# Kernel optimization log

Measured on AMD Instinct MI355X. Metric: run time of the kernel, lower is better.

The kernel has to match this reference:

```python
import jax, jax.numpy as jnp
import numpy as np
from jax import lax

D_MODEL = 512
D_FIBER = 32
D_CONTROL = 64
MOMENTUM = 0.9


def setup_inputs() -> dict:
    key = jax.random.key(0)
    ks = jax.random.split(key, 7)
    B, S = 8, 4096
    hidden = jax.random.normal(ks[0], (B, S, D_MODEL), dtype=jnp.float32)
    # fiber_proj: Linear(d_model -> d_fiber)
    w_fiber = jax.random.normal(ks[1], (D_MODEL, D_FIBER), dtype=jnp.float32) / np.sqrt(D_MODEL)
    b_fiber = jnp.zeros((D_FIBER,), dtype=jnp.float32)
    # predictor: Linear(d_model+d_fiber -> d_control), GELU, Linear(d_control -> 1), Softplus
    w1 = jax.random.normal(ks[2], (D_MODEL + D_FIBER, D_CONTROL), dtype=jnp.float32) / np.sqrt(D_MODEL + D_FIBER)
    b1 = jnp.zeros((D_CONTROL,), dtype=jnp.float32)
    # nn.init.normal_(weight, std=0.01), zero bias for the last linear
    w2 = 0.01 * jax.random.normal(ks[3], (D_CONTROL, 1), dtype=jnp.float32)
    b2 = jnp.zeros((1,), dtype=jnp.float32)
    lambda_gate = jnp.asarray(1.0, dtype=jnp.float32)
    return {"hidden": hidden, "w_fiber": w_fiber, "b_fiber": b_fiber,
            "w1": w1, "b1": b1, "w2": w2, "b2": b2, "lambda_gate": lambda_gate}


def _ema_scan(delta_h, momentum):
    # field_t = momentum * field_{t-1} + (1-momentum) * delta_h_t, field_{-1}=0.
    # Same math as the original full-length causal conv1d (Toeplitz) form,
    # computed in O(S log S) via an associative scan.
    a = jnp.full_like(delta_h, momentum)
    b = (1.0 - momentum) * delta_h

    def combine(c1, c2):
        a1, b1 = c1
        a2, b2 = c2
        return (a1 * a2, a2 * b1 + b2)

    _, field = lax.associative_scan(combine, (a, b), axis=1)
    return field


def reference(hidden, w_fiber, b_fiber, w1, b1, w2, b2, lambda_gate):
    # hidden: [B, S, D]
    fiber = hidden @ w_fiber + b_fiber                      # [B, S, d_fiber]
    combined = jnp.concatenate([hidden, fiber], axis=-1)    # [B, S, D+d_fiber]
    h = jax.nn.gelu(combined @ w1 + b1, approximate=False)  # [B, S, d_control]
    delta_h = jax.nn.softplus((h @ w2 + b2).squeeze(-1))    # [B, S]
    delta_h = jnp.clip(delta_h, 0.0, 1.0)
    field = _ema_scan(delta_h, MOMENTUM)                    # [B, S]
    field = jnp.clip(field, 0.0, 10.0)
    gate = jax.nn.sigmoid(-lambda_gate * field)             # [B, S]
    return (gate, field, delta_h, fiber)
```

## Files before the change

kernel.cpp:

```cpp
#include <hip/hip_runtime.h>
#include <hip/hip_bf16.h>


#define NTOK  32768
#define SEQ   4096
#define DM    512
#define NC    96
#define TB    64
#define LROW  136

typedef short bf16x8 __attribute__((ext_vector_type(8)));
typedef float f32x4  __attribute__((ext_vector_type(4)));

__device__ __forceinline__ unsigned short f2bf(float f) {
    __hip_bfloat16 h = __float2bfloat16(f);
    return *reinterpret_cast<unsigned short*>(&h);
}

__global__ __launch_bounds__(256)
void prep_kernel(const float* __restrict__ wf,
                 const float* __restrict__ bfb,
                 const float* __restrict__ w1,
                 const float* __restrict__ b1,
                 unsigned short* __restrict__ Wt,
                 float* __restrict__ bc)
{
    int idx = blockIdx.x * 256 + threadIdx.x;
    if (idx < NC * DM) {
        int n = idx >> 9, k = idx & 511;
        float v;
        if (n < 32) {
            v = wf[k * 32 + n];
        } else {
            int c = n - 32;
            v = w1[k * 64 + c];
            for (int f = 0; f < 32; ++f)
                v = fmaf(wf[k * 32 + f], w1[(512 + f) * 64 + c], v);
        }
        Wt[idx] = f2bf(v);
    }
    if (idx < NC) {
        float v;
        if (idx < 32) {
            v = bfb[idx];
        } else {
            int c = idx - 32;
            v = b1[c];
            for (int f = 0; f < 32; ++f)
                v = fmaf(bfb[f], w1[(512 + f) * 64 + c], v);
        }
        bc[idx] = v;
    }
}

__global__ __launch_bounds__(256, 2)
void fused_gemm_kernel(const float* __restrict__ hidden,
                       const unsigned short* __restrict__ Wt,
                       const float* __restrict__ bc,
                       const float* __restrict__ w2,
                       const float* __restrict__ b2,
                       float* __restrict__ out_delta,
                       float* __restrict__ out_fiber)
{
    __shared__ unsigned short b_lds[NC * LROW];

    const int tid  = threadIdx.x;
    const int wave = tid >> 6;
    const int lane = tid & 63;
    const int quad = lane >> 4;
    const int l15  = lane & 15;
    const int tok0 = blockIdx.x * TB;

    const float* aptr = hidden + (size_t)(tok0 + wave * 16 + l15) * DM + quad * 8;
    bf16x8 afrag[16];
#pragma unroll
    for (int half = 0; half < 2; ++half) {
        float4 raw[16];
#pragma unroll
        for (int i = 0; i < 16; ++i)
            raw[i] = *(const float4*)(aptr + half * 256 + (i >> 1) * 32 + (i & 1) * 4);
#pragma unroll
        for (int ks = 0; ks < 8; ++ks) {
            float4 lo = raw[ks * 2], hi = raw[ks * 2 + 1];
            bf16x8 f;
            f[0] = (short)f2bf(lo.x); f[1] = (short)f2bf(lo.y);
            f[2] = (short)f2bf(lo.z); f[3] = (short)f2bf(lo.w);
            f[4] = (short)f2bf(hi.x); f[5] = (short)f2bf(hi.y);
            f[6] = (short)f2bf(hi.z); f[7] = (short)f2bf(hi.w);
            afrag[half * 8 + ks] = f;
        }
    }

    f32x4 acc[6];
#pragma unroll
    for (int t = 0; t < 6; ++t) acc[t] = (f32x4){0.f, 0.f, 0.f, 0.f};

    for (int kc = 0; kc < 4; ++kc) {
#pragma unroll
        for (int it = 0; it < 6; ++it) {
            int v   = it * 256 + tid;
            int row = v >> 4;
            int c8  = v & 15;
            *(bf16x8*)&b_lds[row * LROW + c8 * 8] =
                *(const bf16x8*)(Wt + row * DM + kc * 128 + c8 * 8);
        }
        __syncthreads();

#pragma unroll
        for (int ks = 0; ks < 4; ++ks) {
            bf16x8 af = afrag[kc * 4 + ks];
#pragma unroll
            for (int t = 0; t < 6; ++t) {
                bf16x8 bfv = *(const bf16x8*)&b_lds[(t * 16 + l15) * LROW + ks * 32 + quad * 8];
                acc[t] = __builtin_amdgcn_mfma_f32_16x16x32_bf16(af, bfv, acc[t], 0, 0, 0);
            }
        }
        __syncthreads();
    }

    const int mbase = tok0 + wave * 16 + quad * 4;

#pragma unroll
    for (int t = 0; t < 2; ++t) {
        int col = t * 16 + l15;
        float bias = bc[col];
#pragma unroll
        for (int r = 0; r < 4; ++r)
            out_fiber[(size_t)(mbase + r) * 32 + col] = acc[t][r] + bias;
    }

    float p0 = 0.f, p1 = 0.f, p2 = 0.f, p3 = 0.f;
#pragma unroll
    for (int t = 2; t < 6; ++t) {
        int c = (t - 2) * 16 + l15;
        float bias = bc[32 + c];
        float w2v  = w2[c];
        float x, g;
        x = acc[t][0] + bias; g = 0.5f * x * (1.f + erff(x * 0.70710678118f)); p0 = fmaf(g, w2v, p0);
        x = acc[t][1] + bias; g = 0.5f * x * (1.f + erff(x * 0.70710678118f)); p1 = fmaf(g, w2v, p1);
        x = acc[t][2] + bias; g = 0.5f * x * (1.f + erff(x * 0.70710678118f)); p2 = fmaf(g, w2v, p2);
        x = acc[t][3] + bias; g = 0.5f * x * (1.f + erff(x * 0.70710678118f)); p3 = fmaf(g, w2v, p3);
    }
#pragma unroll
    for (int m = 1; m <= 8; m <<= 1) {
        p0 += __shfl_xor(p0, m);
        p1 += __shfl_xor(p1, m);
        p2 += __shfl_xor(p2, m);
        p3 += __shfl_xor(p3, m);
    }
    if (l15 < 4) {
        float pv = (l15 == 0) ? p0 : (l15 == 1) ? p1 : (l15 == 2) ? p2 : p3;
        float s = pv + b2[0];
        float d = (s > 0.f) ? s + log1pf(expf(-s)) : log1pf(expf(s));
        d = fminf(fmaxf(d, 0.f), 1.f);
        out_delta[mbase + l15] = d;
    }
}

__global__ __launch_bounds__(512)
void scan_kernel(const float* __restrict__ delta,
                 const float* __restrict__ lam,
                 float* __restrict__ out_gate,
                 float* __restrict__ out_field)
{
    __shared__ float sA[8], sB[8];
    const int b    = blockIdx.x;
    const int tid  = threadIdx.x;
    const int lane = tid & 63;
    const int wv   = tid >> 6;

    const float* dp = delta + (size_t)b * SEQ + tid * 8;
    float4 d0 = *(const float4*)dp;
    float4 d1 = *(const float4*)(dp + 4);
    float d[8] = {d0.x, d0.y, d0.z, d0.w, d1.x, d1.y, d1.z, d1.w};

    float x = 0.f;
#pragma unroll
    for (int j = 0; j < 8; ++j) x = fmaf(0.9f, x, 0.1f * d[j]);
    float A = 0.430467196f;
    float B = x;

#pragma unroll
    for (int m = 1; m <= 32; m <<= 1) {
        float Au = __shfl_up(A, m);
        float Bu = __shfl_up(B, m);
        if (lane >= m) { B = fmaf(A, Bu, B); A *= Au; }
    }
    if (lane == 63) { sA[wv] = A; sB[wv] = B; }
    __syncthreads();

    float cA = 1.f, cB = 0.f;
    for (int i = 0; i < wv; ++i) { cB = fmaf(sA[i], cB, sB[i]); cA *= sA[i]; }

    float Ap = __shfl_up(A, 1);
    float Bp = __shfl_up(B, 1);
    float f0 = (lane == 0) ? cB : fmaf(Ap, cB, Bp);

    const float lamv = lam[0];
    float xx = f0;
    float4 of0, of1, og0, og1;
    float* ofp = &of0.x;
    float* ogp = &og0.x;
#pragma unroll
    for (int j = 0; j < 8; ++j) {
        xx = fmaf(0.9f, xx, 0.1f * d[j]);
        float field = fminf(fmaxf(xx, 0.f), 10.f);
        float gate  = 1.f / (1.f + expf(lamv * field));
        if (j < 4) { (&of0.x)[j] = field; (&og0.x)[j] = gate; }
        else       { (&of1.x)[j - 4] = field; (&og1.x)[j - 4] = gate; }
    }
    (void)ofp; (void)ogp; (void)cA;
    size_t o = (size_t)b * SEQ + tid * 8;
    *(float4*)(out_field + o)     = of0;
    *(float4*)(out_field + o + 4) = of1;
    *(float4*)(out_gate  + o)     = og0;
    *(float4*)(out_gate  + o + 4) = og1;
}

extern "C" void kernel_launch(void* const* d_in, const int* in_sizes, int n_in,
                              void* d_out, int out_size, void* d_ws, size_t ws_size,
                              hipStream_t stream)
{
    const float* hidden = (const float*)d_in[0];
    const float* wf     = (const float*)d_in[1];
    const float* bfb    = (const float*)d_in[2];
    const float* w1     = (const float*)d_in[3];
    const float* b1     = (const float*)d_in[4];
    const float* w2     = (const float*)d_in[5];
    const float* b2     = (const float*)d_in[6];
    const float* lam    = (const float*)d_in[7];
    float* out = (float*)d_out;
    float* out_gate  = out;
    float* out_field = out + NTOK;
    float* out_delta = out + 2 * NTOK;
    float* out_fiber = out + 3 * NTOK;

    unsigned short* Wt = (unsigned short*)d_ws;
    float* bc          = (float*)((char*)d_ws + NC * DM * 2);

    hipLaunchKernelGGL(prep_kernel, dim3((NC * DM + 255) / 256), dim3(256), 0, stream,
                       wf, bfb, w1, b1, Wt, bc);
    hipLaunchKernelGGL(fused_gemm_kernel, dim3(NTOK / TB), dim3(256), 0, stream,
                       hidden, Wt, bc, w2, b2, out_delta, out_fiber);
    hipLaunchKernelGGL(scan_kernel, dim3(8), dim3(512), 0, stream,
                       out_delta, lam, out_gate, out_field);
}
```

Baseline: 121.1 us.

## Split GEMM K dimension across two wave groups with LDS reduction

The fused GEMM block grows from 4 to 8 waves. Each half of the waves handles one half of the 512-wide K dimension and holds half as many A fragments in registers, which lowers register pressure and allows more waves in flight to hide the global loads of hidden. Partial accumulators are combined through LDS before the GELU/softplus epilogue, at the cost of an extra barrier, more LDS traffic, and an epilogue that only half the waves run. Unused cA bookkeeping in the scan kernel is also removed.

```diff
diff --git a/kernel.cpp b/kernel.cpp
--- a/kernel.cpp
+++ b/kernel.cpp
@@ -53,7 +53,7 @@
     }
 }
 
-__global__ __launch_bounds__(256, 2)
+__global__ __launch_bounds__(512, 4)
 void fused_gemm_kernel(const float* __restrict__ hidden,
                        const unsigned short* __restrict__ Wt,
                        const float* __restrict__ bc,
@@ -62,32 +62,34 @@
                        float* __restrict__ out_delta,
                        float* __restrict__ out_fiber)
 {
-    __shared__ unsigned short b_lds[NC * LROW];
+    __shared__ __attribute__((aligned(16))) unsigned short b_lds[192 * LROW];
 
     const int tid  = threadIdx.x;
     const int wave = tid >> 6;
     const int lane = tid & 63;
     const int quad = lane >> 4;
     const int l15  = lane & 15;
+    const int mw   = wave & 3;
+    const int kh   = wave >> 2;
     const int tok0 = blockIdx.x * TB;
 
-    const float* aptr = hidden + (size_t)(tok0 + wave * 16 + l15) * DM + quad * 8;
-    bf16x8 afrag[16];
-#pragma unroll
-    for (int half = 0; half < 2; ++half) {
-        float4 raw[16];
-#pragma unroll
-        for (int i = 0; i < 16; ++i)
-            raw[i] = *(const float4*)(aptr + half * 256 + (i >> 1) * 32 + (i & 1) * 4);
-#pragma unroll
-        for (int ks = 0; ks < 8; ++ks) {
-            float4 lo = raw[ks * 2], hi = raw[ks * 2 + 1];
+    const float* aptr = hidden + (size_t)(tok0 + mw * 16 + l15) * DM + kh * 256 + quad * 8;
+    bf16x8 afrag[8];
+#pragma unroll
+    for (int g = 0; g < 2; ++g) {
+        float4 raw[8];
+#pragma unroll
+        for (int i = 0; i < 8; ++i)
+            raw[i] = *(const float4*)(aptr + (g * 4 + (i >> 1)) * 32 + (i & 1) * 4);
+#pragma unroll
+        for (int j = 0; j < 4; ++j) {
+            float4 lo = raw[j * 2], hi = raw[j * 2 + 1];
             bf16x8 f;
             f[0] = (short)f2bf(lo.x); f[1] = (short)f2bf(lo.y);
             f[2] = (short)f2bf(lo.z); f[3] = (short)f2bf(lo.w);
             f[4] = (short)f2bf(hi.x); f[5] = (short)f2bf(hi.y);
             f[6] = (short)f2bf(hi.z); f[7] = (short)f2bf(hi.w);
-            afrag[half * 8 + ks] = f;
+            afrag[g * 4 + j] = f;
         }
     }
 
@@ -95,65 +97,81 @@
 #pragma unroll
     for (int t = 0; t < 6; ++t) acc[t] = (f32x4){0.f, 0.f, 0.f, 0.f};
 
-    for (int kc = 0; kc < 4; ++kc) {
+    for (int s = 0; s < 2; ++s) {
 #pragma unroll
         for (int it = 0; it < 6; ++it) {
-            int v   = it * 256 + tid;
-            int row = v >> 4;
+            int v   = it * 512 + tid;
+            int r   = v >> 4;
             int c8  = v & 15;
-            *(bf16x8*)&b_lds[row * LROW + c8 * 8] =
-                *(const bf16x8*)(Wt + row * DM + kc * 128 + c8 * 8);
+            int khr = (r >= 96) ? 1 : 0;
+            int n   = r - khr * 96;
+            *(bf16x8*)&b_lds[r * LROW + c8 * 8] =
+                *(const bf16x8*)(Wt + n * DM + khr * 256 + s * 128 + c8 * 8);
         }
         __syncthreads();
 
 #pragma unroll
         for (int ks = 0; ks < 4; ++ks) {
-            bf16x8 af = afrag[kc * 4 + ks];
+            bf16x8 af = afrag[s * 4 + ks];
 #pragma unroll
             for (int t = 0; t < 6; ++t) {
-                bf16x8 bfv = *(const bf16x8*)&b_lds[(t * 16 + l15) * LROW + ks * 32 + quad * 8];
-                acc[t] = __builtin_amdgcn_mfma_f32_16x16x32_bf16(af, bfv, acc[t], 0, 0, 0);
+                bf16x8 bv = *(const bf16x8*)&b_lds[(kh * 96 + t * 16 + l15) * LROW + ks * 32 + quad * 8];
+                acc[t] = __builtin_amdgcn_mfma_f32_16x16x32_bf16(af, bv, acc[t], 0, 0, 0);
             }
         }
         __syncthreads();
     }
 
-    const int mbase = tok0 + wave * 16 + quad * 4;
-
-#pragma unroll
-    for (int t = 0; t < 2; ++t) {
-        int col = t * 16 + l15;
-        float bias = bc[col];
-#pragma unroll
-        for (int r = 0; r < 4; ++r)
-            out_fiber[(size_t)(mbase + r) * 32 + col] = acc[t][r] + bias;
-    }
-
-    float p0 = 0.f, p1 = 0.f, p2 = 0.f, p3 = 0.f;
-#pragma unroll
-    for (int t = 2; t < 6; ++t) {
-        int c = (t - 2) * 16 + l15;
-        float bias = bc[32 + c];
-        float w2v  = w2[c];
-        float x, g;
-        x = acc[t][0] + bias; g = 0.5f * x * (1.f + erff(x * 0.70710678118f)); p0 = fmaf(g, w2v, p0);
-        x = acc[t][1] + bias; g = 0.5f * x * (1.f + erff(x * 0.70710678118f)); p1 = fmaf(g, w2v, p1);
-        x = acc[t][2] + bias; g = 0.5f * x * (1.f + erff(x * 0.70710678118f)); p2 = fmaf(g, w2v, p2);
-        x = acc[t][3] + bias; g = 0.5f * x * (1.f + erff(x * 0.70710678118f)); p3 = fmaf(g, w2v, p3);
-    }
-#pragma unroll
-    for (int m = 1; m <= 8; m <<= 1) {
-        p0 += __shfl_xor(p0, m);
-        p1 += __shfl_xor(p1, m);
-        p2 += __shfl_xor(p2, m);
-        p3 += __shfl_xor(p3, m);
-    }
-    if (l15 < 4) {
-        float pv = (l15 == 0) ? p0 : (l15 == 1) ? p1 : (l15 == 2) ? p2 : p3;
-        float s = pv + b2[0];
-        float d = (s > 0.f) ? s + log1pf(expf(-s)) : log1pf(expf(s));
-        d = fminf(fmaxf(d, 0.f), 1.f);
-        out_delta[mbase + l15] = d;
+    f32x4* red = (f32x4*)b_lds;
+    if (kh == 1) {
+#pragma unroll
+        for (int t = 0; t < 6; ++t)
+            red[(mw * 6 + t) * 64 + lane] = acc[t];
+    }
+    __syncthreads();
+
+    if (kh == 0) {
+#pragma unroll
+        for (int t = 0; t < 6; ++t)
+            acc[t] = acc[t] + red[(mw * 6 + t) * 64 + lane];
+
+        const int mbase = tok0 + mw * 16 + quad * 4;
+
+#pragma unroll
+        for (int t = 0; t < 2; ++t) {
+            int col = t * 16 + l15;
+            float bias = bc[col];
+#pragma unroll
+            for (int r = 0; r < 4; ++r)
+                out_fiber[(size_t)(mbase + r) * 32 + col] = acc[t][r] + bias;
+        }
+
+        float p0 = 0.f, p1 = 0.f, p2 = 0.f, p3 = 0.f;
+#pragma unroll
+        for (int t = 2; t < 6; ++t) {
+            int c = (t - 2) * 16 + l15;
+            float bias = bc[32 + c];
+            float w2v  = w2[c];
+            float x, g;
+            x = acc[t][0] + bias; g = 0.5f * x * (1.f + erff(x * 0.70710678118f)); p0 = fmaf(g, w2v, p0);
+            x = acc[t][1] + bias; g = 0.5f * x * (1.f + erff(x * 0.70710678118f)); p1 = fmaf(g, w2v, p1);
+            x = acc[t][2] + bias; g = 0.5f * x * (1.f + erff(x * 0.70710678118f)); p2 = fmaf(g, w2v, p2);
+            x = acc[t][3] + bias; g = 0.5f * x * (1.f + erff(x * 0.70710678118f)); p3 = fmaf(g, w2v, p3);
+        }
+#pragma unroll
+        for (int m = 1; m <= 8; m <<= 1) {
+            p0 += __shfl_xor(p0, m);
+            p1 += __shfl_xor(p1, m);
+            p2 += __shfl_xor(p2, m);
+            p3 += __shfl_xor(p3, m);
+        }
+        if (l15 < 4) {
+            float pv = (l15 == 0) ? p0 : (l15 == 1) ? p1 : (l15 == 2) ? p2 : p3;
+            float sft = pv + b2[0];
+            float d = (sft > 0.f) ? sft + log1pf(expf(-sft)) : log1pf(expf(sft));
+            d = fminf(fmaxf(d, 0.f), 1.f);
+            out_delta[mbase + l15] = d;
+        }
     }
 }
 
@@ -189,8 +207,8 @@
     if (lane == 63) { sA[wv] = A; sB[wv] = B; }
     __syncthreads();
 
-    float cA = 1.f, cB = 0.f;
-    for (int i = 0; i < wv; ++i) { cB = fmaf(sA[i], cB, sB[i]); cA *= sA[i]; }
+    float cB = 0.f;
+    for (int i = 0; i < wv; ++i) cB = fmaf(sA[i], cB, sB[i]);
 
     float Ap = __shfl_up(A, 1);
     float Bp = __shfl_up(B, 1);
@@ -199,8 +217,6 @@
     const float lamv = lam[0];
     float xx = f0;
     float4 of0, of1, og0, og1;
-    float* ofp = &of0.x;
-    float* ogp = &og0.x;
 #pragma unroll
     for (int j = 0; j < 8; ++j) {
         xx = fmaf(0.9f, xx, 0.1f * d[j]);
@@ -209,7 +225,6 @@
         if (j < 4) { (&of0.x)[j] = field; (&og0.x)[j] = gate; }
         else       { (&of1.x)[j - 4] = field; (&og1.x)[j - 4] = gate; }
     }
-    (void)ofp; (void)ogp; (void)cA;
     size_t o = (size_t)b * SEQ + tid * 8;
     *(float4*)(out_field + o)     = of0;
     *(float4*)(out_field + o + 4) = of1;
@@ -240,7 +255,7 @@
 
     hipLaunchKernelGGL(prep_kernel, dim3((NC * DM + 255) / 256), dim3(256), 0, stream,
                        wf, bfb, w1, b1, Wt, bc);
-    hipLaunchKernelGGL(fused_gemm_kernel, dim3(NTOK / TB), dim3(256), 0, stream,
+    hipLaunchKernelGGL(fused_gemm_kernel, dim3(NTOK / TB), dim3(512), 0, stream,
                        hidden, Wt, bc, w2, b2, out_delta, out_fiber);
     hipLaunchKernelGGL(scan_kernel, dim3(8), dim3(512), 0, stream,
                        out_delta, lam, out_gate, out_field);
```

New measurement: 118.2 us. -2.4%, faster.
